# Optimization experiments

Measured on AMD Instinct MI355X. Metric: run time of the kernel, lower is better.

Reference implementation:

```python
import jax, jax.numpy as jnp
import numpy as np

B, L, D = 8, 4096, 256
G, K = 64, 8          # n_groups, group_size
N = G * K             # 512 slots
H = 8                 # attention heads
EPS = 1e-5

def _ln(x, g, b):
    m = jnp.mean(x, axis=-1, keepdims=True)
    v = jnp.var(x, axis=-1, keepdims=True)
    return (x - m) * jax.lax.rsqrt(v + EPS) * g + b

def _gelu(x):
    return jax.nn.gelu(x, approximate=False)  # torch nn.GELU default = exact erf

def setup_inputs() -> dict:
    key = jax.random.key(0)
    ks = jax.random.split(key, 24)
    s = 0.02
    d = {
        'X': jax.random.normal(ks[0], (B, L, D), jnp.float32),
        'S': jax.random.normal(ks[1], (B, N, D), jnp.float32),
        'Wg':  jax.random.normal(ks[2], (D, G)) * s,
        'Wk':  jax.random.normal(ks[3], (D, K)) * s,
        'Wm1': jax.random.normal(ks[4], (D, 2*D)) * s, 'bm1': jnp.zeros((2*D,)),
        'Wm2': jax.random.normal(ks[5], (2*D, D)) * s, 'bm2': jnp.zeros((D,)),
        'Wgt1': jax.random.normal(ks[6], (D, D)) * s, 'bgt1': jnp.zeros((D,)),
        'Wgt2': jax.random.normal(ks[7], (D, 1)) * s, 'bgt2': jnp.zeros((1,)),
        'Wqkv': jax.random.normal(ks[8], (D, 3*D)) * s, 'bqkv': jnp.zeros((3*D,)),
        'Wo':  jax.random.normal(ks[9], (D, D)) * s, 'bo': jnp.zeros((D,)),
        'aln_g': jnp.ones((D,)), 'aln_b': jnp.zeros((D,)),
        'Wu1': jax.random.normal(ks[10], (2*D, 2*D)) * s, 'bu1': jnp.zeros((2*D,)),
        'Wu2': jax.random.normal(ks[11], (2*D, D)) * s, 'bu2': jnp.zeros((D,)),
        'ln_g': jnp.ones((D,)), 'ln_b': jnp.zeros((D,)),
    }
    return d

def reference(X, S, Wg, Wk, Wm1, bm1, Wm2, bm2, Wgt1, bgt1, Wgt2, bgt2,
              Wqkv, bqkv, Wo, bo, aln_g, aln_b, Wu1, bu1, Wu2, bu2, ln_g, ln_b):
    # --- hierarchical routing (eval path: argmax one-hot) ---
    msg = _gelu(X @ Wm1 + bm1) @ Wm2 + bm2                 # (B,L,D)
    gate = jax.nn.sigmoid(_gelu(X @ Wgt1 + bgt1) @ Wgt2 + bgt2)  # (B,L,1)
    gm = msg * gate
    gidx = jnp.argmax(X @ Wg, axis=-1)                     # (B,L)
    kidx = jnp.argmax(X @ Wk, axis=-1)                     # (B,L)
    idx = gidx * K + kidx                                  # flat slot id in [0,N)
    full = jax.nn.one_hot(idx, N, dtype=X.dtype)           # (B,L,N)
    incoming = jnp.einsum('bln,bld->bnd', full, gm)        # (B,N,D)
    # --- slot self-attention ---
    qkv = S @ Wqkv + bqkv
    q, k, v = jnp.split(qkv, 3, axis=-1)
    dh = D // H
    q = q.reshape(B, N, H, dh); k = k.reshape(B, N, H, dh); v = v.reshape(B, N, H, dh)
    scores = jnp.einsum('bqhd,bkhd->bhqk', q, k) / jnp.sqrt(jnp.asarray(dh, X.dtype))
    attn = jax.nn.softmax(scores, axis=-1)
    o = jnp.einsum('bhqk,bkhd->bqhd', attn, v).reshape(B, N, D) @ Wo + bo
    S1 = _ln(S + o, aln_g, aln_b)
    # --- update ---
    cat = jnp.concatenate([S1, incoming], axis=-1)         # (B,N,2D)
    S2 = S1 + _gelu(cat @ Wu1 + bu1) @ Wu2 + bu2
    return _ln(S2, ln_g, ln_b)
```

## Files before the change

kernel.cpp:

```cpp
#include <hip/hip_runtime.h>

typedef __bf16 bf16_t;
typedef __bf16 bf16x8 __attribute__((ext_vector_type(8)));
typedef __bf16 bf16x4v __attribute__((ext_vector_type(4)));
typedef __bf16 bf16x2v __attribute__((ext_vector_type(2)));
typedef float f32x4 __attribute__((ext_vector_type(4)));
typedef unsigned long long u64;

#define LN_EPS 1e-5f

__device__ __forceinline__ float erf_fast(float a) {
  const float t = fabsf(a);
  const float s = a * a;
  float r;
  if (t > 0.921875f) {
    float u;
    r = fmaf(-1.72853470e-5f, t, 3.83197126e-4f);
    u = fmaf(-3.88396438e-3f, t, 2.42546219e-2f);
    r = fmaf(r, s, u);
    r = fmaf(r, t, 1.06777877e-1f);
    r = fmaf(r, t, -6.37245935e-1f);
    r = fmaf(r, t, -1.28717512e-1f);
    r = fmaf(r, t, t);
    r = 1.0f - __expf(-r);
    r = copysignf(r, a);
  } else {
    r = -5.96761703e-4f;
    r = fmaf(r, s, 4.99119423e-3f);
    r = fmaf(r, s, -2.67681349e-2f);
    r = fmaf(r, s, 1.12819925e-1f);
    r = fmaf(r, s, -3.76125336e-1f);
    r = fmaf(r, s, 1.28379166e-1f);
    r = fmaf(r, a, a);
  }
  return r;
}

__device__ __forceinline__ float gelu_f(float x) {
  const float h = 0.5f * x;
  return fmaf(h, erf_fast(x * 0.70710678118654752f), h);
}

__device__ __forceinline__ void async16(const bf16_t* g, bf16_t* l) {
  __builtin_amdgcn_global_load_lds(
      (const __attribute__((address_space(1))) void*)g,
      (__attribute__((address_space(3))) void*)l, 16, 0, 0);
}

__device__ __forceinline__ int swz(int row, int p) { return p ^ ((row >> 1) & 3); }

__global__ __launch_bounds__(256)
void prep_kernel(const float* __restrict__ X, const float* __restrict__ S,
                 const float* __restrict__ Wg, const float* __restrict__ Wk,
                 const float* __restrict__ Wm1, const float* __restrict__ Wgt1,
                 const float* __restrict__ Wm2, const float* __restrict__ Wqkv,
                 const float* __restrict__ Wo, const float* __restrict__ Wu1,
                 const float* __restrict__ Wu2,
                 bf16_t* __restrict__ Xb, bf16_t* __restrict__ Sb,
                 bf16_t* __restrict__ W1t, bf16_t* __restrict__ W2t,
                 bf16_t* __restrict__ Wqkvt, bf16_t* __restrict__ Wot,
                 bf16_t* __restrict__ Wu1t, bf16_t* __restrict__ Wu2t,
                 float4* __restrict__ zbase)
{
  const int bid = blockIdx.x;
  const int t = threadIdx.x;
  __shared__ float sT[64][65];

  auto do_tr = [&](const float* src, int C, bf16_t* dst, int ld, int tiles_c, int j) {
    const int r0 = (j / tiles_c) * 64, c0 = (j % tiles_c) * 64;
#pragma unroll 4
    for (int i = 0; i < 16; ++i) {
      const int rr = i * 4 + (t >> 6), cc = t & 63;
      sT[rr][cc] = src[(size_t)(r0 + rr) * C + c0 + cc];
    }
    __syncthreads();
#pragma unroll 4
    for (int i = 0; i < 16; ++i) {
      const int rr = i * 4 + (t >> 6), cc = t & 63;
      dst[(size_t)(c0 + rr) * ld + r0 + cc] = (bf16_t)sT[cc][rr];
    }
  };

  if (bid < 8192) {
    const int i = bid * 256 + t;
    const float4 v = ((const float4*)X)[i];
    bf16x4v o; o[0]=(bf16_t)v.x; o[1]=(bf16_t)v.y; o[2]=(bf16_t)v.z; o[3]=(bf16_t)v.w;
    ((bf16x4v*)Xb)[i] = o;
  } else if (bid < 9216) {
    const int i = (bid - 8192) * 256 + t;
    const float4 v = ((const float4*)S)[i];
    bf16x4v o; o[0]=(bf16_t)v.x; o[1]=(bf16_t)v.y; o[2]=(bf16_t)v.z; o[3]=(bf16_t)v.w;
    ((bf16x4v*)Sb)[i] = o;
  } else if (bid < 9248) {
    do_tr(Wm1, 512, W1t, 256, 8, bid - 9216);
  } else if (bid < 9264) {
    do_tr(Wgt1, 256, W1t + 512 * 256, 256, 4, bid - 9248);
  } else if (bid < 9268) {
    do_tr(Wg, 64, W1t + 768 * 256, 256, 1, bid - 9264);
  } else if (bid < 9269) {
#pragma unroll
    for (int i = 0; i < 8; ++i)
      W1t[(832 + i) * 256 + t] = (bf16_t)Wk[t * 8 + i];
    for (int r = 0; r < 56; ++r)
      W1t[(840 + r) * 256 + t] = (bf16_t)0.f;
  } else if (bid < 9301) {
    do_tr(Wm2, 256, W2t, 512, 4, bid - 9269);
  } else if (bid < 9349) {
    do_tr(Wqkv, 768, Wqkvt, 256, 12, bid - 9301);
  } else if (bid < 9365) {
    do_tr(Wo, 256, Wot, 256, 4, bid - 9349);
  } else if (bid < 9429) {
    do_tr(Wu1, 512, Wu1t, 512, 8, bid - 9365);
  } else if (bid < 9461) {
    do_tr(Wu2, 256, Wu2t, 512, 4, bid - 9429);
  } else {
    zbase[(bid - 9461) * 256 + t] = make_float4(0.f, 0.f, 0.f, 0.f);
  }
}

template<int MT, int EPI>
__global__ __launch_bounds__(256)
void gemm_kernel(const bf16_t* __restrict__ A, int lda,
                 const bf16_t* __restrict__ Bt, int K,
                 const float* __restrict__ bias, const float* __restrict__ bias2,
                 void* __restrict__ outp, int ldc,
                 const float* __restrict__ wgt2, float* __restrict__ gatelin,
                 u64* __restrict__ bitmap)
{
  constexpr int BM = MT * 32;
  constexpr int CA = BM * 4;
  const int m0 = blockIdx.x * BM;
  const int by = blockIdx.y;
  const int n0 = by * 128;
  const int t = threadIdx.x;
  const int w = t >> 6;
  const int lane = t & 63;
  const int wr = w >> 1, wc = w & 1;
  const int quad = lane >> 4, l15 = lane & 15;

  __shared__ bf16_t lA[BM * 32];
  __shared__ bf16_t lB[128 * 32];
  __shared__ float sWg[256];
  __shared__ int sKi[BM];

  if constexpr (EPI == 1) {
    if (by >= 4 && by < 6) sWg[t] = wgt2[t];
  }

  f32x4 acc[MT][4];
#pragma unroll
  for (int mt = 0; mt < MT; ++mt)
#pragma unroll
    for (int nt = 0; nt < 4; ++nt)
      acc[mt][nt] = (f32x4){0.f, 0.f, 0.f, 0.f};

  for (int k0 = 0; k0 < K; k0 += 32) {
    if constexpr (CA >= 256) {
#pragma unroll
      for (int i = 0; i < CA / 256; ++i) {
        const int c = i * 256 + t;
        const int row = c >> 2, pp = c & 3;
        async16(A + (size_t)(m0 + row) * lda + k0 + (swz(row, pp) << 3),
                lA + (size_t)(i * 256 + (t & 192)) * 8);
      }
    } else {
      if (t < CA) {
        const int row = t >> 2, pp = t & 3;
        async16(A + (size_t)(m0 + row) * lda + k0 + (swz(row, pp) << 3),
                lA + (size_t)(t & 192) * 8);
      }
    }
#pragma unroll
    for (int i = 0; i < 2; ++i) {
      const int c = i * 256 + t;
      const int row = c >> 2, pp = c & 3;
      async16(Bt + (size_t)(n0 + row) * K + k0 + (swz(row, pp) << 3),
              lB + (size_t)(i * 256 + (t & 192)) * 8);
    }
    __syncthreads();
    bf16x8 af[MT], bfr[4];
#pragma unroll
    for (int mt = 0; mt < MT; ++mt) {
      const int row = wr * MT * 16 + mt * 16 + l15;
      af[mt] = *(const bf16x8*)&lA[row * 32 + (swz(row, quad) << 3)];
    }
#pragma unroll
    for (int nt = 0; nt < 4; ++nt) {
      const int row = wc * 64 + nt * 16 + l15;
      bfr[nt] = *(const bf16x8*)&lB[row * 32 + (swz(row, quad) << 3)];
    }
#pragma unroll
    for (int mt = 0; mt < MT; ++mt)
#pragma unroll
      for (int nt = 0; nt < 4; ++nt)
        acc[mt][nt] = __builtin_amdgcn_mfma_f32_16x16x32_bf16(bfr[nt], af[mt], acc[mt][nt], 0, 0, 0);
    __syncthreads();
  }

  if constexpr (EPI == 1) {
    if (by < 4) {
#pragma unroll
      for (int mt = 0; mt < MT; ++mt) {
        const int row = m0 + wr * MT * 16 + mt * 16 + l15;
#pragma unroll
        for (int nt = 0; nt < 4; ++nt) {
          const int colb = n0 + wc * 64 + nt * 16 + quad * 4;
          const float4 bb = *(const float4*)&bias[colb];
          bf16x4v o;
          o[0] = (bf16_t)(acc[mt][nt][0] + bb.x);
          o[1] = (bf16_t)(acc[mt][nt][1] + bb.y);
          o[2] = (bf16_t)(acc[mt][nt][2] + bb.z);
          o[3] = (bf16_t)(acc[mt][nt][3] + bb.w);
          *(bf16x4v*)&((bf16_t*)outp)[(size_t)row * 512 + colb] = o;
        }
      }
    } else if (by < 6) {
#pragma unroll
      for (int mt = 0; mt < MT; ++mt) {
        const int row = m0 + wr * MT * 16 + mt * 16 + l15;
        float part = 0.f;
#pragma unroll
        for (int nt = 0; nt < 4; ++nt) {
          const int colb = n0 + wc * 64 + nt * 16 + quad * 4;
          const int c = colb - 512;
          const float4 bb = *(const float4*)&bias2[c];
          part = fmaf(gelu_f(acc[mt][nt][0] + bb.x), sWg[c + 0], part);
          part = fmaf(gelu_f(acc[mt][nt][1] + bb.y), sWg[c + 1], part);
          part = fmaf(gelu_f(acc[mt][nt][2] + bb.z), sWg[c + 2], part);
          part = fmaf(gelu_f(acc[mt][nt][3] + bb.w), sWg[c + 3], part);
        }
        part += __shfl_xor(part, 16, 64);
        part += __shfl_xor(part, 32, 64);
        if (lane < 16) atomicAdd(&gatelin[row], part);
      }
    } else {
      int bi[MT];
#pragma unroll
      for (int mt = 0; mt < MT; ++mt) {
        if (wc == 0) {
          float mv = -1e30f; int mi = 0;
#pragma unroll
          for (int nt = 0; nt < 4; ++nt)
#pragma unroll
            for (int j = 0; j < 4; ++j) {
              const int gc = nt * 16 + quad * 4 + j;
              const float v = acc[mt][nt][j];
              if (v > mv || (v == mv && gc < mi)) { mv = v; mi = gc; }
            }
#pragma unroll
          for (int off = 16; off <= 32; off <<= 1) {
            const float ov = __shfl_xor(mv, off, 64);
            const int oi = __shfl_xor(mi, off, 64);
            if (ov > mv || (ov == mv && oi < mi)) { mv = ov; mi = oi; }
          }
          bi[mt] = mi;
        } else {
          float mv = -1e30f; int mi = 0;
          if (quad < 2) {
#pragma unroll
            for (int j = 0; j < 4; ++j) {
              const int kc = quad * 4 + j;
              const float v = acc[mt][0][j];
              if (v > mv || (v == mv && kc < mi)) { mv = v; mi = kc; }
            }
          }
#pragma unroll
          for (int off = 16; off <= 32; off <<= 1) {
            const float ov = __shfl_xor(mv, off, 64);
            const int oi = __shfl_xor(mi, off, 64);
            if (ov > mv || (ov == mv && oi < mi)) { mv = ov; mi = oi; }
          }
          if (lane < 16) sKi[wr * MT * 16 + mt * 16 + l15] = mi;
        }
      }
      __syncthreads();
      if (wc == 0 && lane < 16) {
#pragma unroll
        for (int mt = 0; mt < MT; ++mt) {
          const int rl = wr * MT * 16 + mt * 16 + l15;
          const int row = m0 + rl;
          const int idx = bi[mt] * 8 + sKi[rl];
          const int b = row >> 12, tok = row & 4095;
          atomicOr(&bitmap[(size_t)(b * 512 + idx) * 64 + (tok >> 6)],
                   1ull << (tok & 63));
        }
      }
    }
  }
}

__global__ __launch_bounds__(256)
void gemm_pair_kernel(const bf16_t* __restrict__ H, const bf16_t* __restrict__ W2t,
                      const float* __restrict__ bm2, const float* __restrict__ sumg,
                      float* __restrict__ incom,
                      const bf16_t* __restrict__ Sb, const bf16_t* __restrict__ Wqkvt,
                      const float* __restrict__ bqkv, bf16_t* __restrict__ qkvb)
{
  int id = blockIdx.x;
  const bool first = id < 256;
  if (!first) id -= 256;
  const bf16_t* A  = first ? H : Sb;
  const bf16_t* Bt = first ? W2t : Wqkvt;
  const float* bias = first ? bm2 : bqkv;
  const int lda = first ? 512 : 256;
  const int K   = first ? 512 : 256;
  const int ldc = first ? 256 : 768;
  const int m0 = (id & 127) * 32;
  const int n0 = (id >> 7) * 128;
  const int t = threadIdx.x;
  const int w = t >> 6;
  const int lane = t & 63;
  const int wr = w >> 1, wc = w & 1;
  const int quad = lane >> 4, l15 = lane & 15;

  __shared__ bf16_t lA[32 * 32];
  __shared__ bf16_t lB[128 * 32];

  f32x4 acc[4];
#pragma unroll
  for (int nt = 0; nt < 4; ++nt) acc[nt] = (f32x4){0.f, 0.f, 0.f, 0.f};

  for (int k0 = 0; k0 < K; k0 += 32) {
    if (t < 128) {
      const int row = t >> 2, pp = t & 3;
      async16(A + (size_t)(m0 + row) * lda + k0 + (swz(row, pp) << 3),
              lA + (size_t)(t & 192) * 8);
    }
#pragma unroll
    for (int i = 0; i < 2; ++i) {
      const int c = i * 256 + t;
      const int row = c >> 2, pp = c & 3;
      async16(Bt + (size_t)(n0 + row) * K + k0 + (swz(row, pp) << 3),
              lB + (size_t)(i * 256 + (t & 192)) * 8);
    }
    __syncthreads();
    bf16x8 af, bfr[4];
    const int arow = wr * 16 + l15;
    af = *(const bf16x8*)&lA[arow * 32 + (swz(arow, quad) << 3)];
#pragma unroll
    for (int nt = 0; nt < 4; ++nt) {
      const int row = wc * 64 + nt * 16 + l15;
      bfr[nt] = *(const bf16x8*)&lB[row * 32 + (swz(row, quad) << 3)];
    }
#pragma unroll
    for (int nt = 0; nt < 4; ++nt)
      acc[nt] = __builtin_amdgcn_mfma_f32_16x16x32_bf16(bfr[nt], af, acc[nt], 0, 0, 0);
    __syncthreads();
  }

  const int row = m0 + wr * 16 + l15;
  if (first) {
    const float gt = sumg[row];
#pragma unroll
    for (int nt = 0; nt < 4; ++nt) {
      const int colb = n0 + wc * 64 + nt * 16 + quad * 4;
      const float4 bb = *(const float4*)&bias[colb];
      *(float4*)&incom[(size_t)row * ldc + colb] =
          make_float4(fmaf(gt, bb.x, acc[nt][0]), fmaf(gt, bb.y, acc[nt][1]),
                      fmaf(gt, bb.z, acc[nt][2]), fmaf(gt, bb.w, acc[nt][3]));
    }
  } else {
#pragma unroll
    for (int nt = 0; nt < 4; ++nt) {
      const int colb = n0 + wc * 64 + nt * 16 + quad * 4;
      const float4 bb = *(const float4*)&bias[colb];
      bf16x4v o; o[0]=(bf16_t)(acc[nt][0]+bb.x); o[1]=(bf16_t)(acc[nt][1]+bb.y);
      o[2]=(bf16_t)(acc[nt][2]+bb.z); o[3]=(bf16_t)(acc[nt][3]+bb.w);
      *(bf16x4v*)&qkvb[(size_t)row * ldc + colb] = o;
    }
  }
}

__global__ __launch_bounds__(256)
void gather_kernel(const bf16_t* __restrict__ h1, const float* __restrict__ gatelin,
                   const float* __restrict__ bgt2, const u64* __restrict__ bitmap,
                   bf16_t* __restrict__ H, float* __restrict__ sumg)
{
  const int bs = blockIdx.x;
  const int b = bs >> 9;
  const int t = threadIdx.x;
  __shared__ u64 sw[64];
  if (t < 64) sw[t] = bitmap[(size_t)bs * 64 + t];
  __syncthreads();
  const float bg = bgt2[0];
  float a0 = 0.f, a1 = 0.f, sg = 0.f;
  for (int wd = 0; wd < 64; ++wd) {
    u64 word = sw[wd];
    while (word) {
      const int bit = __builtin_ctzll(word);
      word &= word - 1;
      const int l = (b << 12) + (wd << 6) + bit;
      const float g = 1.0f / (1.0f + __expf(-(gatelin[l] + bg)));
      const bf16x2v hv = *(const bf16x2v*)&h1[(size_t)l * 512 + t * 2];
      a0 = fmaf(g, gelu_f((float)hv[0]), a0);
      a1 = fmaf(g, gelu_f((float)hv[1]), a1);
      sg += g;
    }
  }
  bf16x2v o; o[0] = (bf16_t)a0; o[1] = (bf16_t)a1;
  *(bf16x2v*)&H[(size_t)bs * 512 + t * 2] = o;
  if (t == 0) sumg[bs] = sg;
}

__global__ __launch_bounds__(256)
void attn_kernel(const bf16_t* __restrict__ qkv, bf16_t* __restrict__ obuf)
{
  const int bid = blockIdx.x;
  const int qc = bid & 15;
  const int h = (bid >> 4) & 7;
  const int b = bid >> 7;
  const int t = threadIdx.x;
  const int w = t >> 6, lane = t & 63;
  const int quad = lane >> 4, l15 = lane & 15;

  __shared__ bf16_t sP[32 * 520];
  __shared__ bf16_t sVt[32 * 264];
  __shared__ float sL[32];

  bf16x8 qf[2];
#pragma unroll
  for (int mt = 0; mt < 2; ++mt) {
    const int row = b * 512 + qc * 32 + mt * 16 + l15;
    qf[mt] = *(const bf16x8*)&qkv[(size_t)row * 768 + h * 32 + quad * 8];
  }
  const float scale = 0.17677669529663687f;
  for (int kt = w; kt < 32; kt += 4) {
    const int key = b * 512 + kt * 16 + l15;
    const bf16x8 kf = *(const bf16x8*)&qkv[(size_t)key * 768 + 256 + h * 32 + quad * 8];
#pragma unroll
    for (int mt = 0; mt < 2; ++mt) {
      f32x4 c = (f32x4){0.f, 0.f, 0.f, 0.f};
      c = __builtin_amdgcn_mfma_f32_16x16x32_bf16(qf[mt], kf, c, 0, 0, 0);
#pragma unroll
      for (int r = 0; r < 4; ++r)
        sP[(mt * 16 + quad * 4 + r) * 520 + kt * 16 + l15] = (bf16_t)(c[r] * scale);
    }
  }
  __syncthreads();

#pragma unroll
  for (int ri = 0; ri < 8; ++ri) {
    const int row = w * 8 + ri;
    const bf16x8 sv = *(const bf16x8*)&sP[row * 520 + lane * 8];
    float sval[8];
    float mx = -1e30f;
#pragma unroll
    for (int j = 0; j < 8; ++j) { sval[j] = (float)sv[j]; mx = fmaxf(mx, sval[j]); }
#pragma unroll
    for (int off = 32; off; off >>= 1) mx = fmaxf(mx, __shfl_xor(mx, off, 64));
    float sum = 0.f;
    bf16x8 pv;
#pragma unroll
    for (int j = 0; j < 8; ++j) { const float e = __expf(sval[j] - mx); sum += e; pv[j] = (bf16_t)e; }
#pragma unroll
    for (int off = 32; off; off >>= 1) sum += __shfl_xor(sum, off, 64);
    *(bf16x8*)&sP[row * 520 + lane * 8] = pv;
    if (lane == 0) sL[row] = sum;
  }
  __syncthreads();

  const int omt = w >> 1, ont = w & 1;
  f32x4 oacc = (f32x4){0.f, 0.f, 0.f, 0.f};
  for (int half = 0; half < 2; ++half) {
    if (half) __syncthreads();
#pragma unroll
    for (int i = 0; i < 32; ++i) {
      const int el = i * 256 + t;
      const int dh = el & 31, key = el >> 5;
      sVt[dh * 264 + key] = qkv[(size_t)(b * 512 + half * 256 + key) * 768 + 512 + h * 32 + dh];
    }
    __syncthreads();
#pragma unroll
    for (int kt = 0; kt < 8; ++kt) {
      const bf16x8 af = *(const bf16x8*)&sP[(omt * 16 + l15) * 520 + half * 256 + kt * 32 + quad * 8];
      const bf16x8 vf = *(const bf16x8*)&sVt[(ont * 16 + l15) * 264 + kt * 32 + quad * 8];
      oacc = __builtin_amdgcn_mfma_f32_16x16x32_bf16(af, vf, oacc, 0, 0, 0);
    }
  }
#pragma unroll
  for (int r = 0; r < 4; ++r) {
    const int row = omt * 16 + quad * 4 + r;
    const float val = oacc[r] / sL[row];
    obuf[(size_t)(b * 512 + qc * 32 + row) * 256 + h * 32 + ont * 16 + l15] = (bf16_t)val;
  }
}

__global__ __launch_bounds__(256)
void slot_tail_kernel(const bf16_t* __restrict__ obuf, const bf16_t* __restrict__ Wot,
                      const float* __restrict__ bo, const float* __restrict__ S,
                      const float* __restrict__ incom,
                      const float* __restrict__ ag, const float* __restrict__ ab,
                      const bf16_t* __restrict__ Wu1t, const float* __restrict__ bu1,
                      const bf16_t* __restrict__ Wu2t, const float* __restrict__ bu2,
                      const float* __restrict__ lg, const float* __restrict__ lb,
                      float* __restrict__ out)
{
  const int m0 = blockIdx.x * 16;
  const int t = threadIdx.x;
  const int w = t >> 6, lane = t & 63;
  const int quad = lane >> 4, l15 = lane & 15;

  __shared__ bf16_t lB[512 * 32];
  __shared__ bf16_t lA[16 * 32];
  __shared__ bf16_t sA[16 * 520];
  __shared__ float sSum[4][16], sSq[4][16];

  f32x4 acc[4];
#pragma unroll
  for (int nt = 0; nt < 4; ++nt) acc[nt] = (f32x4){0.f, 0.f, 0.f, 0.f};
  for (int k0 = 0; k0 < 256; k0 += 32) {
    if (t < 64) {
      const int row = t >> 2, pp = t & 3;
      async16(obuf + (size_t)(m0 + row) * 256 + k0 + (swz(row, pp) << 3), lA);
    }
#pragma unroll
    for (int i = 0; i < 4; ++i) {
      const int c = i * 256 + t;
      const int row = c >> 2, pp = c & 3;
      async16(Wot + (size_t)row * 256 + k0 + (swz(row, pp) << 3),
              lB + (size_t)(i * 256 + (t & 192)) * 8);
    }
    __syncthreads();
    const bf16x8 af = *(const bf16x8*)&lA[l15 * 32 + (swz(l15, quad) << 3)];
#pragma unroll
    for (int nt = 0; nt < 4; ++nt) {
      const int row = w * 64 + nt * 16 + l15;
      const bf16x8 bfr = *(const bf16x8*)&lB[row * 32 + (swz(row, quad) << 3)];
      acc[nt] = __builtin_amdgcn_mfma_f32_16x16x32_bf16(bfr, af, acc[nt], 0, 0, 0);
    }
    __syncthreads();
  }

  const int row = m0 + l15;
  float sum = 0.f, sq = 0.f;
#pragma unroll
  for (int nt = 0; nt < 4; ++nt) {
    const int colb = w * 64 + nt * 16 + quad * 4;
    const float4 bv = *(const float4*)&bo[colb];
    const float4 sv = *(const float4*)&S[(size_t)row * 256 + colb];
    float x0 = acc[nt][0] + bv.x + sv.x, x1 = acc[nt][1] + bv.y + sv.y;
    float x2 = acc[nt][2] + bv.z + sv.z, x3 = acc[nt][3] + bv.w + sv.w;
    acc[nt][0] = x0; acc[nt][1] = x1; acc[nt][2] = x2; acc[nt][3] = x3;
    sum += x0 + x1 + x2 + x3;
    sq += x0*x0 + x1*x1 + x2*x2 + x3*x3;
  }
  sum += __shfl_xor(sum, 16, 64); sum += __shfl_xor(sum, 32, 64);
  sq  += __shfl_xor(sq, 16, 64);  sq  += __shfl_xor(sq, 32, 64);
  if (lane < 16) { sSum[w][l15] = sum; sSq[w][l15] = sq; }
  __syncthreads();
  {
    const float tot = sSum[0][l15] + sSum[1][l15] + sSum[2][l15] + sSum[3][l15];
    const float tq  = sSq[0][l15] + sSq[1][l15] + sSq[2][l15] + sSq[3][l15];
    const float mean = tot * 0.00390625f;
    const float var = tq * 0.00390625f - mean * mean;
    const float rstd = rsqrtf(var + LN_EPS);
#pragma unroll
    for (int nt = 0; nt < 4; ++nt) {
      const int colb = w * 64 + nt * 16 + quad * 4;
      const float4 gg = *(const float4*)&ag[colb];
      const float4 bv = *(const float4*)&ab[colb];
      acc[nt][0] = (acc[nt][0]-mean)*rstd*gg.x + bv.x;
      acc[nt][1] = (acc[nt][1]-mean)*rstd*gg.y + bv.y;
      acc[nt][2] = (acc[nt][2]-mean)*rstd*gg.z + bv.z;
      acc[nt][3] = (acc[nt][3]-mean)*rstd*gg.w + bv.w;
      bf16x4v yb; yb[0]=(bf16_t)acc[nt][0]; yb[1]=(bf16_t)acc[nt][1];
      yb[2]=(bf16_t)acc[nt][2]; yb[3]=(bf16_t)acc[nt][3];
      *(bf16x4v*)&sA[l15 * 520 + colb] = yb;
    }
  }
#pragma unroll
  for (int i = 0; i < 16; ++i) {
    const int idx = i * 256 + t;
    const int rr = idx >> 8, cc = idx & 255;
    sA[rr * 520 + 256 + cc] = (bf16_t)incom[(size_t)(m0 + rr) * 256 + cc];
  }
  float y[16];
#pragma unroll
  for (int nt = 0; nt < 4; ++nt)
#pragma unroll
    for (int j = 0; j < 4; ++j) y[nt * 4 + j] = acc[nt][j];
  __syncthreads();

  f32x4 acc2[8];
#pragma unroll
  for (int nt = 0; nt < 8; ++nt) acc2[nt] = (f32x4){0.f, 0.f, 0.f, 0.f};
  for (int k0 = 0; k0 < 512; k0 += 32) {
#pragma unroll
    for (int i = 0; i < 8; ++i) {
      const int c = i * 256 + t;
      const int rown = c >> 2, pp = c & 3;
      async16(Wu1t + (size_t)rown * 512 + k0 + (swz(rown, pp) << 3),
              lB + (size_t)(i * 256 + (t & 192)) * 8);
    }
    __syncthreads();
    const bf16x8 af = *(const bf16x8*)&sA[l15 * 520 + k0 + quad * 8];
#pragma unroll
    for (int nt = 0; nt < 8; ++nt) {
      const int rown = w * 128 + nt * 16 + l15;
      const bf16x8 bfr = *(const bf16x8*)&lB[rown * 32 + (swz(rown, quad) << 3)];
      acc2[nt] = __builtin_amdgcn_mfma_f32_16x16x32_bf16(bfr, af, acc2[nt], 0, 0, 0);
    }
    __syncthreads();
  }
#pragma unroll
  for (int nt = 0; nt < 8; ++nt) {
    const int colb = w * 128 + nt * 16 + quad * 4;
    const float4 bv = *(const float4*)&bu1[colb];
    bf16x4v o;
    o[0] = (bf16_t)gelu_f(acc2[nt][0] + bv.x);
    o[1] = (bf16_t)gelu_f(acc2[nt][1] + bv.y);
    o[2] = (bf16_t)gelu_f(acc2[nt][2] + bv.z);
    o[3] = (bf16_t)gelu_f(acc2[nt][3] + bv.w);
    *(bf16x4v*)&sA[l15 * 520 + colb] = o;
  }
  __syncthreads();

  f32x4 acc3[4];
#pragma unroll
  for (int nt = 0; nt < 4; ++nt) acc3[nt] = (f32x4){0.f, 0.f, 0.f, 0.f};
  for (int k0 = 0; k0 < 512; k0 += 32) {
#pragma unroll
    for (int i = 0; i < 4; ++i) {
      const int c = i * 256 + t;
      const int rown = c >> 2, pp = c & 3;
      async16(Wu2t + (size_t)rown * 512 + k0 + (swz(rown, pp) << 3),
              lB + (size_t)(i * 256 + (t & 192)) * 8);
    }
    __syncthreads();
    const bf16x8 af = *(const bf16x8*)&sA[l15 * 520 + k0 + quad * 8];
#pragma unroll
    for (int nt = 0; nt < 4; ++nt) {
      const int rown = w * 64 + nt * 16 + l15;
      const bf16x8 bfr = *(const bf16x8*)&lB[rown * 32 + (swz(rown, quad) << 3)];
      acc3[nt] = __builtin_amdgcn_mfma_f32_16x16x32_bf16(bfr, af, acc3[nt], 0, 0, 0);
    }
    __syncthreads();
  }
  float sum2 = 0.f, sq2 = 0.f;
#pragma unroll
  for (int nt = 0; nt < 4; ++nt) {
    const int colb = w * 64 + nt * 16 + quad * 4;
    const float4 bv = *(const float4*)&bu2[colb];
    float x0 = acc3[nt][0] + bv.x + y[nt*4+0], x1 = acc3[nt][1] + bv.y + y[nt*4+1];
    float x2 = acc3[nt][2] + bv.z + y[nt*4+2], x3 = acc3[nt][3] + bv.w + y[nt*4+3];
    acc3[nt][0] = x0; acc3[nt][1] = x1; acc3[nt][2] = x2; acc3[nt][3] = x3;
    sum2 += x0 + x1 + x2 + x3;
    sq2 += x0*x0 + x1*x1 + x2*x2 + x3*x3;
  }
  sum2 += __shfl_xor(sum2, 16, 64); sum2 += __shfl_xor(sum2, 32, 64);
  sq2  += __shfl_xor(sq2, 16, 64);  sq2  += __shfl_xor(sq2, 32, 64);
  if (lane < 16) { sSum[w][l15] = sum2; sSq[w][l15] = sq2; }
  __syncthreads();
  const float tot2 = sSum[0][l15] + sSum[1][l15] + sSum[2][l15] + sSum[3][l15];
  const float tq2  = sSq[0][l15] + sSq[1][l15] + sSq[2][l15] + sSq[3][l15];
  const float mean2 = tot2 * 0.00390625f;
  const float var2 = tq2 * 0.00390625f - mean2 * mean2;
  const float rstd2 = rsqrtf(var2 + LN_EPS);
#pragma unroll
  for (int nt = 0; nt < 4; ++nt) {
    const int colb = w * 64 + nt * 16 + quad * 4;
    const float4 gg = *(const float4*)&lg[colb];
    const float4 bv = *(const float4*)&lb[colb];
    *(float4*)&out[(size_t)row * 256 + colb] = make_float4(
        (acc3[nt][0]-mean2)*rstd2*gg.x + bv.x, (acc3[nt][1]-mean2)*rstd2*gg.y + bv.y,
        (acc3[nt][2]-mean2)*rstd2*gg.z + bv.z, (acc3[nt][3]-mean2)*rstd2*gg.w + bv.w);
  }
}

extern "C" void kernel_launch(void* const* d_in, const int* in_sizes, int n_in,
                              void* d_out, int out_size, void* d_ws, size_t ws_size,
                              hipStream_t stream)
{
  (void)in_sizes; (void)n_in; (void)out_size; (void)ws_size;
  const float* X    = (const float*)d_in[0];
  const float* S    = (const float*)d_in[1];
  const float* Wg   = (const float*)d_in[2];
  const float* Wk   = (const float*)d_in[3];
  const float* Wm1  = (const float*)d_in[4];
  const float* bm1  = (const float*)d_in[5];
  const float* Wm2  = (const float*)d_in[6];
  const float* bm2  = (const float*)d_in[7];
  const float* Wgt1 = (const float*)d_in[8];
  const float* bgt1 = (const float*)d_in[9];
  const float* Wgt2 = (const float*)d_in[10];
  const float* bgt2 = (const float*)d_in[11];
  const float* Wqkv = (const float*)d_in[12];
  const float* bqkv = (const float*)d_in[13];
  const float* Wo   = (const float*)d_in[14];
  const float* bo   = (const float*)d_in[15];
  const float* alng = (const float*)d_in[16];
  const float* alnb = (const float*)d_in[17];
  const float* Wu1  = (const float*)d_in[18];
  const float* bu1  = (const float*)d_in[19];
  const float* Wu2  = (const float*)d_in[20];
  const float* bu2  = (const float*)d_in[21];
  const float* lng  = (const float*)d_in[22];
  const float* lnb  = (const float*)d_in[23];

  char* p = (char*)d_ws;
  auto carve = [&](size_t bytes) { char* r = p; p += bytes; return r; };
  bf16_t* Xb    = (bf16_t*)carve(16777216);
  bf16_t* Sb    = (bf16_t*)carve(2097152);
  bf16_t* W1t   = (bf16_t*)carve(458752);
  bf16_t* W2t   = (bf16_t*)carve(262144);
  bf16_t* Wqkvt = (bf16_t*)carve(393216);
  bf16_t* Wot   = (bf16_t*)carve(131072);
  bf16_t* Wu1t  = (bf16_t*)carve(524288);
  bf16_t* Wu2t  = (bf16_t*)carve(262144);
  bf16_t* h1    = (bf16_t*)carve(33554432);
  u64*    bitmap  = (u64*)carve(2097152);
  float*  gatelin = (float*)carve(131072);
  float*  incom = (float*)carve(4194304);
  bf16_t* qkvb  = (bf16_t*)carve(6291456);
  bf16_t* obuf  = (bf16_t*)carve(2097152);
  bf16_t* H     = (bf16_t*)carve(4194304);
  float*  sumg  = (float*)carve(16384);

  prep_kernel<<<10005, 256, 0, stream>>>(X, S, Wg, Wk, Wm1, Wgt1, Wm2, Wqkv, Wo, Wu1, Wu2,
                                         Xb, Sb, W1t, W2t, Wqkvt, Wot, Wu1t, Wu2t,
                                         (float4*)bitmap);
  gemm_kernel<2,1><<<dim3(512,7), 256, 0, stream>>>(Xb, 256, W1t, 256, bm1, bgt1, h1, 512,
                                                    Wgt2, gatelin, bitmap);
  gather_kernel<<<4096, 256, 0, stream>>>(h1, gatelin, bgt2, bitmap, H, sumg);
  gemm_pair_kernel<<<1024, 256, 0, stream>>>(H, W2t, bm2, sumg, incom,
                                             Sb, Wqkvt, bqkv, qkvb);
  attn_kernel<<<1024, 256, 0, stream>>>(qkvb, obuf);
  slot_tail_kernel<<<256, 256, 0, stream>>>(obuf, Wot, bo, S, incom, alng, alnb,
                                            Wu1t, bu1, Wu2t, bu2, lng, lnb,
                                            (float*)d_out);
}
```

Before: 263.4 us.

## Merge kernels: fold QKV GEMM into first GEMM, attention with gather, Wm2 into tail

The QKV projection moves into the first routing GEMM launch as an extra grid row, and the gather and attention kernels become one launch split by block index. The Wm2 message projection moves into the slot tail kernel, which computes the incoming rows in shared memory instead of reading an fp32 incom buffer. This cuts the launch count from six to four, adds more independent blocks per launch, and removes the incom round trip through global memory. In exchange the tail kernel does an extra K=512 GEMM with only 256 blocks, and the shared-memory footprint of the merged kernels rises.

```diff
diff --git a/kernel.cpp b/kernel.cpp
--- a/kernel.cpp
+++ b/kernel.cpp
@@ -118,70 +118,63 @@
   }
 }
 
-template<int MT, int EPI>
 __global__ __launch_bounds__(256)
-void gemm_kernel(const bf16_t* __restrict__ A, int lda,
-                 const bf16_t* __restrict__ Bt, int K,
-                 const float* __restrict__ bias, const float* __restrict__ bias2,
-                 void* __restrict__ outp, int ldc,
-                 const float* __restrict__ wgt2, float* __restrict__ gatelin,
-                 u64* __restrict__ bitmap)
+void g1r_kernel(const bf16_t* __restrict__ Xb, const bf16_t* __restrict__ W1t,
+                const float* __restrict__ bm1, const float* __restrict__ bgt1,
+                bf16_t* __restrict__ h1,
+                const float* __restrict__ wgt2, float* __restrict__ gatelin,
+                u64* __restrict__ bitmap,
+                const bf16_t* __restrict__ Sb, const bf16_t* __restrict__ Wqkvt,
+                const float* __restrict__ bqkv, bf16_t* __restrict__ qkvb)
 {
-  constexpr int BM = MT * 32;
-  constexpr int CA = BM * 4;
-  const int m0 = blockIdx.x * BM;
   const int by = blockIdx.y;
-  const int n0 = by * 128;
+  const bool isqkv = (by == 7);
+  if (isqkv && blockIdx.x >= 384) return;
+
+  const bf16_t* Ap = isqkv ? Sb : Xb;
+  const bf16_t* Btp = isqkv ? Wqkvt : W1t;
+  const int m0 = isqkv ? (blockIdx.x & 63) * 64 : blockIdx.x * 64;
+  const int n0 = isqkv ? (blockIdx.x >> 6) * 128 : by * 128;
   const int t = threadIdx.x;
   const int w = t >> 6;
   const int lane = t & 63;
   const int wr = w >> 1, wc = w & 1;
   const int quad = lane >> 4, l15 = lane & 15;
 
-  __shared__ bf16_t lA[BM * 32];
+  __shared__ bf16_t lA[64 * 32];
   __shared__ bf16_t lB[128 * 32];
   __shared__ float sWg[256];
-  __shared__ int sKi[BM];
-
-  if constexpr (EPI == 1) {
-    if (by >= 4 && by < 6) sWg[t] = wgt2[t];
-  }
-
-  f32x4 acc[MT][4];
-#pragma unroll
-  for (int mt = 0; mt < MT; ++mt)
+  __shared__ int sKi[64];
+
+  if (by >= 4 && by < 6) sWg[t] = wgt2[t];
+
+  f32x4 acc[2][4];
+#pragma unroll
+  for (int mt = 0; mt < 2; ++mt)
 #pragma unroll
     for (int nt = 0; nt < 4; ++nt)
       acc[mt][nt] = (f32x4){0.f, 0.f, 0.f, 0.f};
 
-  for (int k0 = 0; k0 < K; k0 += 32) {
-    if constexpr (CA >= 256) {
-#pragma unroll
-      for (int i = 0; i < CA / 256; ++i) {
-        const int c = i * 256 + t;
-        const int row = c >> 2, pp = c & 3;
-        async16(A + (size_t)(m0 + row) * lda + k0 + (swz(row, pp) << 3),
-                lA + (size_t)(i * 256 + (t & 192)) * 8);
-      }
-    } else {
-      if (t < CA) {
-        const int row = t >> 2, pp = t & 3;
-        async16(A + (size_t)(m0 + row) * lda + k0 + (swz(row, pp) << 3),
-                lA + (size_t)(t & 192) * 8);
-      }
-    }
+  for (int k0 = 0; k0 < 256; k0 += 32) {
 #pragma unroll
     for (int i = 0; i < 2; ++i) {
       const int c = i * 256 + t;
       const int row = c >> 2, pp = c & 3;
-      async16(Bt + (size_t)(n0 + row) * K + k0 + (swz(row, pp) << 3),
+      async16(Ap + (size_t)(m0 + row) * 256 + k0 + (swz(row, pp) << 3),
+              lA + (size_t)(i * 256 + (t & 192)) * 8);
+    }
+#pragma unroll
+    for (int i = 0; i < 2; ++i) {
+      const int c = i * 256 + t;
+      const int row = c >> 2, pp = c & 3;
+      async16(Btp + (size_t)(n0 + row) * 256 + k0 + (swz(row, pp) << 3),
               lB + (size_t)(i * 256 + (t & 192)) * 8);
     }
     __syncthreads();
-    bf16x8 af[MT], bfr[4];
-#pragma unroll
-    for (int mt = 0; mt < MT; ++mt) {
-      const int row = wr * MT * 16 + mt * 16 + l15;
+    bf16x8 af[2], bfr[4];
+#pragma unroll
+    for (int mt = 0; mt < 2; ++mt) {
+      const int row = wr * 32 + mt * 16 + l15;
       af[mt] = *(const bf16x8*)&lA[row * 32 + (swz(row, quad) << 3)];
     }
 #pragma unroll
@@ -190,232 +183,162 @@
       bfr[nt] = *(const bf16x8*)&lB[row * 32 + (swz(row, quad) << 3)];
     }
 #pragma unroll
-    for (int mt = 0; mt < MT; ++mt)
+    for (int mt = 0; mt < 2; ++mt)
 #pragma unroll
       for (int nt = 0; nt < 4; ++nt)
         acc[mt][nt] = __builtin_amdgcn_mfma_f32_16x16x32_bf16(bfr[nt], af[mt], acc[mt][nt], 0, 0, 0);
     __syncthreads();
   }
 
-  if constexpr (EPI == 1) {
-    if (by < 4) {
-#pragma unroll
-      for (int mt = 0; mt < MT; ++mt) {
-        const int row = m0 + wr * MT * 16 + mt * 16 + l15;
-#pragma unroll
-        for (int nt = 0; nt < 4; ++nt) {
-          const int colb = n0 + wc * 64 + nt * 16 + quad * 4;
-          const float4 bb = *(const float4*)&bias[colb];
-          bf16x4v o;
-          o[0] = (bf16_t)(acc[mt][nt][0] + bb.x);
-          o[1] = (bf16_t)(acc[mt][nt][1] + bb.y);
-          o[2] = (bf16_t)(acc[mt][nt][2] + bb.z);
-          o[3] = (bf16_t)(acc[mt][nt][3] + bb.w);
-          *(bf16x4v*)&((bf16_t*)outp)[(size_t)row * 512 + colb] = o;
+  if (isqkv) {
+#pragma unroll
+    for (int mt = 0; mt < 2; ++mt) {
+      const int row = m0 + wr * 32 + mt * 16 + l15;
+#pragma unroll
+      for (int nt = 0; nt < 4; ++nt) {
+        const int colb = n0 + wc * 64 + nt * 16 + quad * 4;
+        const float4 bb = *(const float4*)&bqkv[colb];
+        bf16x4v o;
+        o[0]=(bf16_t)(acc[mt][nt][0]+bb.x); o[1]=(bf16_t)(acc[mt][nt][1]+bb.y);
+        o[2]=(bf16_t)(acc[mt][nt][2]+bb.z); o[3]=(bf16_t)(acc[mt][nt][3]+bb.w);
+        *(bf16x4v*)&qkvb[(size_t)row * 768 + colb] = o;
+      }
+    }
+  } else if (by < 4) {
+#pragma unroll
+    for (int mt = 0; mt < 2; ++mt) {
+      const int row = m0 + wr * 32 + mt * 16 + l15;
+#pragma unroll
+      for (int nt = 0; nt < 4; ++nt) {
+        const int colb = n0 + wc * 64 + nt * 16 + quad * 4;
+        const float4 bb = *(const float4*)&bm1[colb];
+        bf16x4v o;
+        o[0] = (bf16_t)(acc[mt][nt][0] + bb.x);
+        o[1] = (bf16_t)(acc[mt][nt][1] + bb.y);
+        o[2] = (bf16_t)(acc[mt][nt][2] + bb.z);
+        o[3] = (bf16_t)(acc[mt][nt][3] + bb.w);
+        *(bf16x4v*)&h1[(size_t)row * 512 + colb] = o;
+      }
+    }
+  } else if (by < 6) {
+#pragma unroll
+    for (int mt = 0; mt < 2; ++mt) {
+      const int row = m0 + wr * 32 + mt * 16 + l15;
+      float part = 0.f;
+#pragma unroll
+      for (int nt = 0; nt < 4; ++nt) {
+        const int colb = n0 + wc * 64 + nt * 16 + quad * 4;
+        const int c = colb - 512;
+        const float4 bb = *(const float4*)&bgt1[c];
+        part = fmaf(gelu_f(acc[mt][nt][0] + bb.x), sWg[c + 0], part);
+        part = fmaf(gelu_f(acc[mt][nt][1] + bb.y), sWg[c + 1], part);
+        part = fmaf(gelu_f(acc[mt][nt][2] + bb.z), sWg[c + 2], part);
+        part = fmaf(gelu_f(acc[mt][nt][3] + bb.w), sWg[c + 3], part);
+      }
+      part += __shfl_xor(part, 16, 64);
+      part += __shfl_xor(part, 32, 64);
+      if (lane < 16) atomicAdd(&gatelin[row], part);
+    }
+  } else {
+    int bi[2];
+#pragma unroll
+    for (int mt = 0; mt < 2; ++mt) {
+      if (wc == 0) {
+        float mv = -1e30f; int mi = 0;
+#pragma unroll
+        for (int nt = 0; nt < 4; ++nt)
+#pragma unroll
+          for (int j = 0; j < 4; ++j) {
+            const int gc = nt * 16 + quad * 4 + j;
+            const float v = acc[mt][nt][j];
+            if (v > mv || (v == mv && gc < mi)) { mv = v; mi = gc; }
+          }
+#pragma unroll
+        for (int off = 16; off <= 32; off <<= 1) {
+          const float ov = __shfl_xor(mv, off, 64);
+          const int oi = __shfl_xor(mi, off, 64);
+          if (ov > mv || (ov == mv && oi < mi)) { mv = ov; mi = oi; }
         }
+        bi[mt] = mi;
+      } else {
+        float mv = -1e30f; int mi = 0;
+        if (quad < 2) {
+#pragma unroll
+          for (int j = 0; j < 4; ++j) {
+            const int kc = quad * 4 + j;
+            const float v = acc[mt][0][j];
+            if (v > mv || (v == mv && kc < mi)) { mv = v; mi = kc; }
+          }
+        }
+#pragma unroll
+        for (int off = 16; off <= 32; off <<= 1) {
+          const float ov = __shfl_xor(mv, off, 64);
+          const int oi = __shfl_xor(mi, off, 64);
+          if (ov > mv || (ov == mv && oi < mi)) { mv = ov; mi = oi; }
+        }
+        if (lane < 16) sKi[wr * 32 + mt * 16 + l15] = mi;
       }
-    } else if (by < 6) {
-#pragma unroll
-      for (int mt = 0; mt < MT; ++mt) {
-        const int row = m0 + wr * MT * 16 + mt * 16 + l15;
-        float part = 0.f;
-#pragma unroll
-        for (int nt = 0; nt < 4; ++nt) {
-          const int colb = n0 + wc * 64 + nt * 16 + quad * 4;
-          const int c = colb - 512;
-          const float4 bb = *(const float4*)&bias2[c];
-          part = fmaf(gelu_f(acc[mt][nt][0] + bb.x), sWg[c + 0], part);
-          part = fmaf(gelu_f(acc[mt][nt][1] + bb.y), sWg[c + 1], part);
-          part = fmaf(gelu_f(acc[mt][nt][2] + bb.z), sWg[c + 2], part);
-          part = fmaf(gelu_f(acc[mt][nt][3] + bb.w), sWg[c + 3], part);
-        }
-        part += __shfl_xor(part, 16, 64);
-        part += __shfl_xor(part, 32, 64);
-        if (lane < 16) atomicAdd(&gatelin[row], part);
+    }
+    __syncthreads();
+    if (wc == 0 && lane < 16) {
+#pragma unroll
+      for (int mt = 0; mt < 2; ++mt) {
+        const int rl = wr * 32 + mt * 16 + l15;
+        const int row = m0 + rl;
+        const int idx = bi[mt] * 8 + sKi[rl];
+        const int b = row >> 12, tok = row & 4095;
+        atomicOr(&bitmap[(size_t)(b * 512 + idx) * 64 + (tok >> 6)],
+                 1ull << (tok & 63));
       }
-    } else {
-      int bi[MT];
-#pragma unroll
-      for (int mt = 0; mt < MT; ++mt) {
-        if (wc == 0) {
-          float mv = -1e30f; int mi = 0;
-#pragma unroll
-          for (int nt = 0; nt < 4; ++nt)
-#pragma unroll
-            for (int j = 0; j < 4; ++j) {
-              const int gc = nt * 16 + quad * 4 + j;
-              const float v = acc[mt][nt][j];
-              if (v > mv || (v == mv && gc < mi)) { mv = v; mi = gc; }
-            }
-#pragma unroll
-          for (int off = 16; off <= 32; off <<= 1) {
-            const float ov = __shfl_xor(mv, off, 64);
-            const int oi = __shfl_xor(mi, off, 64);
-            if (ov > mv || (ov == mv && oi < mi)) { mv = ov; mi = oi; }
-          }
-          bi[mt] = mi;
-        } else {
-          float mv = -1e30f; int mi = 0;
-          if (quad < 2) {
-#pragma unroll
-            for (int j = 0; j < 4; ++j) {
-              const int kc = quad * 4 + j;
-              const float v = acc[mt][0][j];
-              if (v > mv || (v == mv && kc < mi)) { mv = v; mi = kc; }
-            }
-          }
-#pragma unroll
-          for (int off = 16; off <= 32; off <<= 1) {
-            const float ov = __shfl_xor(mv, off, 64);
-            const int oi = __shfl_xor(mi, off, 64);
-            if (ov > mv || (ov == mv && oi < mi)) { mv = ov; mi = oi; }
-          }
-          if (lane < 16) sKi[wr * MT * 16 + mt * 16 + l15] = mi;
-        }
+    }
+  }
+}
+
+__global__ __launch_bounds__(256)
+void mid_kernel(const bf16_t* __restrict__ h1, const float* __restrict__ gatelin,
+                const float* __restrict__ bgt2, const u64* __restrict__ bitmap,
+                bf16_t* __restrict__ H, float* __restrict__ sumg,
+                const bf16_t* __restrict__ qkv, bf16_t* __restrict__ obuf)
+{
+  __shared__ bf16_t sP[32 * 520];
+  __shared__ bf16_t sVt[32 * 264];
+  __shared__ float sL[32];
+  __shared__ u64 sw[64];
+
+  const int t = threadIdx.x;
+
+  if (blockIdx.x < 4096) {
+    const int bs = blockIdx.x;
+    const int b = bs >> 9;
+    if (t < 64) sw[t] = bitmap[(size_t)bs * 64 + t];
+    __syncthreads();
+    const float bg = bgt2[0];
+    float a0 = 0.f, a1 = 0.f, sg = 0.f;
+    for (int wd = 0; wd < 64; ++wd) {
+      u64 word = sw[wd];
+      while (word) {
+        const int bit = __builtin_ctzll(word);
+        word &= word - 1;
+        const int l = (b << 12) + (wd << 6) + bit;
+        const float g = 1.0f / (1.0f + __expf(-(gatelin[l] + bg)));
+        const bf16x2v hv = *(const bf16x2v*)&h1[(size_t)l * 512 + t * 2];
+        a0 = fmaf(g, gelu_f((float)hv[0]), a0);
+        a1 = fmaf(g, gelu_f((float)hv[1]), a1);
+        sg += g;
       }
-      __syncthreads();
-      if (wc == 0 && lane < 16) {
-#pragma unroll
-        for (int mt = 0; mt < MT; ++mt) {
-          const int rl = wr * MT * 16 + mt * 16 + l15;
-          const int row = m0 + rl;
-          const int idx = bi[mt] * 8 + sKi[rl];
-          const int b = row >> 12, tok = row & 4095;
-          atomicOr(&bitmap[(size_t)(b * 512 + idx) * 64 + (tok >> 6)],
-                   1ull << (tok & 63));
-        }
-      }
-    }
-  }
-}
-
-__global__ __launch_bounds__(256)
-void gemm_pair_kernel(const bf16_t* __restrict__ H, const bf16_t* __restrict__ W2t,
-                      const float* __restrict__ bm2, const float* __restrict__ sumg,
-                      float* __restrict__ incom,
-                      const bf16_t* __restrict__ Sb, const bf16_t* __restrict__ Wqkvt,
-                      const float* __restrict__ bqkv, bf16_t* __restrict__ qkvb)
-{
-  int id = blockIdx.x;
-  const bool first = id < 256;
-  if (!first) id -= 256;
-  const bf16_t* A  = first ? H : Sb;
-  const bf16_t* Bt = first ? W2t : Wqkvt;
-  const float* bias = first ? bm2 : bqkv;
-  const int lda = first ? 512 : 256;
-  const int K   = first ? 512 : 256;
-  const int ldc = first ? 256 : 768;
-  const int m0 = (id & 127) * 32;
-  const int n0 = (id >> 7) * 128;
-  const int t = threadIdx.x;
-  const int w = t >> 6;
-  const int lane = t & 63;
-  const int wr = w >> 1, wc = w & 1;
-  const int quad = lane >> 4, l15 = lane & 15;
-
-  __shared__ bf16_t lA[32 * 32];
-  __shared__ bf16_t lB[128 * 32];
-
-  f32x4 acc[4];
-#pragma unroll
-  for (int nt = 0; nt < 4; ++nt) acc[nt] = (f32x4){0.f, 0.f, 0.f, 0.f};
-
-  for (int k0 = 0; k0 < K; k0 += 32) {
-    if (t < 128) {
-      const int row = t >> 2, pp = t & 3;
-      async16(A + (size_t)(m0 + row) * lda + k0 + (swz(row, pp) << 3),
-              lA + (size_t)(t & 192) * 8);
-    }
-#pragma unroll
-    for (int i = 0; i < 2; ++i) {
-      const int c = i * 256 + t;
-      const int row = c >> 2, pp = c & 3;
-      async16(Bt + (size_t)(n0 + row) * K + k0 + (swz(row, pp) << 3),
-              lB + (size_t)(i * 256 + (t & 192)) * 8);
-    }
-    __syncthreads();
-    bf16x8 af, bfr[4];
-    const int arow = wr * 16 + l15;
-    af = *(const bf16x8*)&lA[arow * 32 + (swz(arow, quad) << 3)];
-#pragma unroll
-    for (int nt = 0; nt < 4; ++nt) {
-      const int row = wc * 64 + nt * 16 + l15;
-      bfr[nt] = *(const bf16x8*)&lB[row * 32 + (swz(row, quad) << 3)];
-    }
-#pragma unroll
-    for (int nt = 0; nt < 4; ++nt)
-      acc[nt] = __builtin_amdgcn_mfma_f32_16x16x32_bf16(bfr[nt], af, acc[nt], 0, 0, 0);
-    __syncthreads();
-  }
-
-  const int row = m0 + wr * 16 + l15;
-  if (first) {
-    const float gt = sumg[row];
-#pragma unroll
-    for (int nt = 0; nt < 4; ++nt) {
-      const int colb = n0 + wc * 64 + nt * 16 + quad * 4;
-      const float4 bb = *(const float4*)&bias[colb];
-      *(float4*)&incom[(size_t)row * ldc + colb] =
-          make_float4(fmaf(gt, bb.x, acc[nt][0]), fmaf(gt, bb.y, acc[nt][1]),
-                      fmaf(gt, bb.z, acc[nt][2]), fmaf(gt, bb.w, acc[nt][3]));
-    }
-  } else {
-#pragma unroll
-    for (int nt = 0; nt < 4; ++nt) {
-      const int colb = n0 + wc * 64 + nt * 16 + quad * 4;
-      const float4 bb = *(const float4*)&bias[colb];
-      bf16x4v o; o[0]=(bf16_t)(acc[nt][0]+bb.x); o[1]=(bf16_t)(acc[nt][1]+bb.y);
-      o[2]=(bf16_t)(acc[nt][2]+bb.z); o[3]=(bf16_t)(acc[nt][3]+bb.w);
-      *(bf16x4v*)&qkvb[(size_t)row * ldc + colb] = o;
-    }
-  }
-}
-
-__global__ __launch_bounds__(256)
-void gather_kernel(const bf16_t* __restrict__ h1, const float* __restrict__ gatelin,
-                   const float* __restrict__ bgt2, const u64* __restrict__ bitmap,
-                   bf16_t* __restrict__ H, float* __restrict__ sumg)
-{
-  const int bs = blockIdx.x;
-  const int b = bs >> 9;
-  const int t = threadIdx.x;
-  __shared__ u64 sw[64];
-  if (t < 64) sw[t] = bitmap[(size_t)bs * 64 + t];
-  __syncthreads();
-  const float bg = bgt2[0];
-  float a0 = 0.f, a1 = 0.f, sg = 0.f;
-  for (int wd = 0; wd < 64; ++wd) {
-    u64 word = sw[wd];
-    while (word) {
-      const int bit = __builtin_ctzll(word);
-      word &= word - 1;
-      const int l = (b << 12) + (wd << 6) + bit;
-      const float g = 1.0f / (1.0f + __expf(-(gatelin[l] + bg)));
-      const bf16x2v hv = *(const bf16x2v*)&h1[(size_t)l * 512 + t * 2];
-      a0 = fmaf(g, gelu_f((float)hv[0]), a0);
-      a1 = fmaf(g, gelu_f((float)hv[1]), a1);
-      sg += g;
-    }
-  }
-  bf16x2v o; o[0] = (bf16_t)a0; o[1] = (bf16_t)a1;
-  *(bf16x2v*)&H[(size_t)bs * 512 + t * 2] = o;
-  if (t == 0) sumg[bs] = sg;
-}
-
-__global__ __launch_bounds__(256)
-void attn_kernel(const bf16_t* __restrict__ qkv, bf16_t* __restrict__ obuf)
-{
-  const int bid = blockIdx.x;
+    }
+    bf16x2v o; o[0] = (bf16_t)a0; o[1] = (bf16_t)a1;
+    *(bf16x2v*)&H[(size_t)bs * 512 + t * 2] = o;
+    if (t == 0) sumg[bs] = sg;
+    return;
+  }
+
+  const int bid = blockIdx.x - 4096;
   const int qc = bid & 15;
   const int h = (bid >> 4) & 7;
   const int b = bid >> 7;
-  const int t = threadIdx.x;
   const int w = t >> 6, lane = t & 63;
   const int quad = lane >> 4, l15 = lane & 15;
-
-  __shared__ bf16_t sP[32 * 520];
-  __shared__ bf16_t sVt[32 * 264];
-  __shared__ float sL[32];
 
   bf16x8 qf[2];
 #pragma unroll
@@ -488,7 +411,8 @@
 __global__ __launch_bounds__(256)
 void slot_tail_kernel(const bf16_t* __restrict__ obuf, const bf16_t* __restrict__ Wot,
                       const float* __restrict__ bo, const float* __restrict__ S,
-                      const float* __restrict__ incom,
+                      const bf16_t* __restrict__ H, const bf16_t* __restrict__ W2t,
+                      const float* __restrict__ bm2, const float* __restrict__ sumg,
                       const float* __restrict__ ag, const float* __restrict__ ab,
                       const bf16_t* __restrict__ Wu1t, const float* __restrict__ bu1,
                       const bf16_t* __restrict__ Wu2t, const float* __restrict__ bu2,
@@ -506,6 +430,45 @@
   __shared__ float sSum[4][16], sSq[4][16];
 
   f32x4 acc[4];
+#pragma unroll
+  for (int nt = 0; nt < 4; ++nt) acc[nt] = (f32x4){0.f, 0.f, 0.f, 0.f};
+  for (int k0 = 0; k0 < 512; k0 += 32) {
+    if (t < 64) {
+      const int row = t >> 2, pp = t & 3;
+      async16(H + (size_t)(m0 + row) * 512 + k0 + (swz(row, pp) << 3), lA);
+    }
+#pragma unroll
+    for (int i = 0; i < 4; ++i) {
+      const int c = i * 256 + t;
+      const int row = c >> 2, pp = c & 3;
+      async16(W2t + (size_t)row * 512 + k0 + (swz(row, pp) << 3),
+              lB + (size_t)(i * 256 + (t & 192)) * 8);
+    }
+    __syncthreads();
+    const bf16x8 af = *(const bf16x8*)&lA[l15 * 32 + (swz(l15, quad) << 3)];
+#pragma unroll
+    for (int nt = 0; nt < 4; ++nt) {
+      const int row = w * 64 + nt * 16 + l15;
+      const bf16x8 bfr = *(const bf16x8*)&lB[row * 32 + (swz(row, quad) << 3)];
+      acc[nt] = __builtin_amdgcn_mfma_f32_16x16x32_bf16(bfr, af, acc[nt], 0, 0, 0);
+    }
+    __syncthreads();
+  }
+  {
+    const float gt = sumg[m0 + l15];
+#pragma unroll
+    for (int nt = 0; nt < 4; ++nt) {
+      const int colb = w * 64 + nt * 16 + quad * 4;
+      const float4 bb = *(const float4*)&bm2[colb];
+      bf16x4v o;
+      o[0] = (bf16_t)fmaf(gt, bb.x, acc[nt][0]);
+      o[1] = (bf16_t)fmaf(gt, bb.y, acc[nt][1]);
+      o[2] = (bf16_t)fmaf(gt, bb.z, acc[nt][2]);
+      o[3] = (bf16_t)fmaf(gt, bb.w, acc[nt][3]);
+      *(bf16x4v*)&sA[l15 * 520 + 256 + colb] = o;
+    }
+  }
+
 #pragma unroll
   for (int nt = 0; nt < 4; ++nt) acc[nt] = (f32x4){0.f, 0.f, 0.f, 0.f};
   for (int k0 = 0; k0 < 256; k0 += 32) {
@@ -567,12 +530,6 @@
       yb[2]=(bf16_t)acc[nt][2]; yb[3]=(bf16_t)acc[nt][3];
       *(bf16x4v*)&sA[l15 * 520 + colb] = yb;
     }
-  }
-#pragma unroll
-  for (int i = 0; i < 16; ++i) {
-    const int idx = i * 256 + t;
-    const int rr = idx >> 8, cc = idx & 255;
-    sA[rr * 520 + 256 + cc] = (bf16_t)incom[(size_t)(m0 + rr) * 256 + cc];
   }
   float y[16];
 #pragma unroll
@@ -710,7 +667,6 @@
   bf16_t* h1    = (bf16_t*)carve(33554432);
   u64*    bitmap  = (u64*)carve(2097152);
   float*  gatelin = (float*)carve(131072);
-  float*  incom = (float*)carve(4194304);
   bf16_t* qkvb  = (bf16_t*)carve(6291456);
   bf16_t* obuf  = (bf16_t*)carve(2097152);
   bf16_t* H     = (bf16_t*)carve(4194304);
@@ -719,13 +675,10 @@
   prep_kernel<<<10005, 256, 0, stream>>>(X, S, Wg, Wk, Wm1, Wgt1, Wm2, Wqkv, Wo, Wu1, Wu2,
                                          Xb, Sb, W1t, W2t, Wqkvt, Wot, Wu1t, Wu2t,
                                          (float4*)bitmap);
-  gemm_kernel<2,1><<<dim3(512,7), 256, 0, stream>>>(Xb, 256, W1t, 256, bm1, bgt1, h1, 512,
-                                                    Wgt2, gatelin, bitmap);
-  gather_kernel<<<4096, 256, 0, stream>>>(h1, gatelin, bgt2, bitmap, H, sumg);
-  gemm_pair_kernel<<<1024, 256, 0, stream>>>(H, W2t, bm2, sumg, incom,
-                                             Sb, Wqkvt, bqkv, qkvb);
-  attn_kernel<<<1024, 256, 0, stream>>>(qkvb, obuf);
-  slot_tail_kernel<<<256, 256, 0, stream>>>(obuf, Wot, bo, S, incom, alng, alnb,
-                                            Wu1t, bu1, Wu2t, bu2, lng, lnb,
+  g1r_kernel<<<dim3(512, 8), 256, 0, stream>>>(Xb, W1t, bm1, bgt1, h1, Wgt2, gatelin,
+                                               bitmap, Sb, Wqkvt, bqkv, qkvb);
+  mid_kernel<<<5120, 256, 0, stream>>>(h1, gatelin, bgt2, bitmap, H, sumg, qkvb, obuf);
+  slot_tail_kernel<<<256, 256, 0, stream>>>(obuf, Wot, bo, S, H, W2t, bm2, sumg,
+                                            alng, alnb, Wu1t, bu1, Wu2t, bu2, lng, lnb,
                                             (float*)d_out);
 }
```

After: 283.1 us. 7.5% more time.
